# Performance work log

Measured on AMD Instinct MI355X. Metric: run time of the kernel, lower is better.

The kernel has to match this reference:

```python
import jax, jax.numpy as jnp
import numpy as np

N = 4096     # num nodes
FEAT = 500   # knn attribute dim
HID = 512    # args.hid_dim
E = 65536    # edges (avg degree 16)
T = 8        # args.time -> euler steps with step_size=1


def setup_inputs() -> dict:
    key = jax.random.key(0)
    ks = jax.random.split(key, 10)
    knn = jax.random.normal(ks[0], (N, FEAT), jnp.float32)
    adj = jax.random.uniform(ks[1], (N, N), jnp.float32)
    norm_factor = jnp.ones((), jnp.float32)
    edge_index = jax.random.randint(ks[2], (2, E), 0, N, dtype=jnp.int32).astype(jnp.int64)
    edge_weight = jax.random.uniform(ks[3], (E,), jnp.float32)
    # AGCN params (init eye + small noise so math is non-trivial)
    w1 = jnp.eye(N, dtype=jnp.float32) + 0.01 * jax.random.normal(ks[4], (N, N), jnp.float32)
    w2 = jnp.eye(N, dtype=jnp.float32) + 0.01 * jax.random.normal(ks[5], (N, N), jnp.float32)
    # extractor: Linear(N, HID) then Linear(HID, HID), kaiming-normal (relu), zero bias
    W0 = jax.random.normal(ks[6], (HID, N), jnp.float32) * np.float32((2.0 / N) ** 0.5)
    b0 = jnp.zeros((HID,), jnp.float32)
    W1 = jax.random.normal(ks[7], (HID, HID), jnp.float32) * np.float32((2.0 / HID) ** 0.5)
    b1 = jnp.zeros((HID,), jnp.float32)
    # LaplacianODEFunc scalar params
    alpha_train = jnp.asarray(0.5, jnp.float32)
    beta_train = jnp.asarray(0.1, jnp.float32)
    return dict(knn=knn, adj=adj, norm_factor=norm_factor, w1=w1, w2=w2,
                W0=W0, b0=b0, W1=W1, b1=b1, edge_weight=edge_weight,
                alpha_train=alpha_train, beta_train=beta_train, edge_index=edge_index)


def _spmm(edge_index, edge_weight, x):
    # out[row] += w * x[col], row=edge_index[0], col=edge_index[1]
    msg = edge_weight[:, None] * x[edge_index[1]]          # [E, HID]
    return jax.ops.segment_sum(msg, edge_index[0], num_segments=x.shape[0])


def reference(knn, adj, norm_factor, w1, w2, W0, b0, W1, b1,
              edge_weight, alpha_train, beta_train, edge_index):
    # ---- AGCN ----
    H = (adj @ w1) @ adj.T                                  # [N, N]
    H = (H @ w2) @ knn                                      # [N, FEAT]
    embed = H @ H.T                                         # [N, N]
    norm = jnp.maximum(jnp.linalg.norm(embed, axis=1, keepdims=True), 1e-12)
    embed = embed / norm                                    # F.normalize(dim=1)
    # ---- extractor MLP (no activation in source; dropout=eval no-op) ----
    h = embed @ W0.T + b0                                   # [N, HID]
    h = h @ W1.T + b1                                       # [N, HID]
    # ---- ODE diffusion: dx/dt = sigmoid(a)*(Ax - x) + b*x0, explicit Euler dt=1 ----
    x0 = jax.lax.stop_gradient(h)
    alpha = jax.nn.sigmoid(alpha_train)

    def step(x, _):
        ax = _spmm(edge_index, edge_weight, x)
        return x + alpha * (ax - x) + beta_train * x0, None

    z_ode, _ = jax.lax.scan(step, h, None, length=T)
    z = jax.nn.relu(norm_factor * z_ode + h)
    z = (z - z.mean(0)) / jnp.std(z, ddof=1)                # torch std is unbiased
    return z
```

## Files before the change

### kernel.cpp

```cpp
#include <hip/hip_runtime.h>
#include <stdint.h>
#include <stddef.h>

typedef __bf16 bf16;
typedef __attribute__((ext_vector_type(8))) __bf16 bf16x8;
typedef __attribute__((ext_vector_type(4))) __bf16 bf16x4;
typedef __attribute__((ext_vector_type(4))) float f32x4;

#define NN 4096
#define HIDD 512
#define NE 65536

__device__ inline void gll16(const void* g, void* l) {
    __builtin_amdgcn_global_load_lds(
        (const __attribute__((address_space(1))) void*)g,
        (__attribute__((address_space(3))) void*)l, 16, 0, 0);
}

__global__ void cvt_f32_bf16(const float* __restrict__ in, bf16* __restrict__ out, int n) {
    int i = (blockIdx.x * 256 + threadIdx.x) * 4;
    if (i >= n) return;
    float4 v = *reinterpret_cast<const float4*>(in + i);
    bf16x4 o;
    o[0] = (bf16)v.x; o[1] = (bf16)v.y; o[2] = (bf16)v.z; o[3] = (bf16)v.w;
    *reinterpret_cast<bf16x4*>(out + i) = o;
}

__global__ void reduce_bf16_slices(const bf16* __restrict__ in, bf16* __restrict__ out,
                                   int n, int S) {
    int i = (blockIdx.x * 256 + threadIdx.x) * 8;
    if (i >= n) return;
    float acc[8] = {};
    for (int k = 0; k < S; ++k) {
        bf16x8 v = *reinterpret_cast<const bf16x8*>(in + (size_t)k * n + i);
#pragma unroll
        for (int j = 0; j < 8; ++j) acc[j] += (float)v[j];
    }
    bf16x8 o;
#pragma unroll
    for (int j = 0; j < 8; ++j) o[j] = (bf16)acc[j];
    *reinterpret_cast<bf16x8*>(out + i) = o;
}

__global__ void transpose_pad_f32(const float* __restrict__ in, bf16* __restrict__ out,
                                  int R, int C, int Cpad) {
    __shared__ bf16 tile[32][33];
    int c0 = blockIdx.x * 32, r0 = blockIdx.y * 32;
    int tx = threadIdx.x, ty = threadIdx.y;
    for (int i = ty; i < 32; i += 8) {
        int r = r0 + i, c = c0 + tx;
        bf16 v = (bf16)0.f;
        if (r < R && c < C) v = (bf16)in[(size_t)r * C + c];
        tile[i][tx] = v;
    }
    __syncthreads();
    for (int i = ty; i < 32; i += 8) {
        int oc = c0 + i, orow = r0 + tx;
        if (oc < Cpad && orow < R) out[(size_t)oc * R + orow] = tile[tx][i];
    }
}

__global__ void transpose_bf16(const bf16* __restrict__ in, bf16* __restrict__ out,
                               int R, int C) {
    __shared__ bf16 tile[32][33];
    int c0 = blockIdx.x * 32, r0 = blockIdx.y * 32;
    int tx = threadIdx.x, ty = threadIdx.y;
    for (int i = ty; i < 32; i += 8)
        tile[i][tx] = in[(size_t)(r0 + i) * C + c0 + tx];
    __syncthreads();
    for (int i = ty; i < 32; i += 8)
        out[(size_t)(c0 + i) * R + r0 + tx] = tile[tx][i];
}

template<int OMODE, bool HAS_BIAS, bool ROW_SCALE>
__global__ __launch_bounds__(256)
void gemm_nt(const bf16* __restrict__ A, const bf16* __restrict__ B,
             void* __restrict__ Cp, const float* __restrict__ bias,
             const float* __restrict__ rowscale, int M, int N, int K) {
    __shared__ __align__(16) bf16 As[128 * 32];
    __shared__ __align__(16) bf16 Bs[128 * 32];
    const int tid  = threadIdx.x;
    const int wave = tid >> 6;
    const int lane = tid & 63;
    const int m0 = blockIdx.y * 128, n0 = blockIdx.x * 128;
    const int lrow = lane >> 2;
    const int lcol = (lane & 3) * 8;
    const int c0 = wave * 2;
    const size_t arow0 = (size_t)(m0 + c0 * 16 + lrow) * K + lcol;
    const size_t arow1 = (size_t)(m0 + (c0 + 1) * 16 + lrow) * K + lcol;
    const size_t brow0 = (size_t)(n0 + c0 * 16 + lrow) * K + lcol;
    const size_t brow1 = (size_t)(n0 + (c0 + 1) * 16 + lrow) * K + lcol;
    bf16* asd0 = &As[c0 * 512];
    bf16* asd1 = &As[(c0 + 1) * 512];
    bf16* bsd0 = &Bs[c0 * 512];
    bf16* bsd1 = &Bs[(c0 + 1) * 512];

    f32x4 acc[4][4] = {};

    const int wm = (wave >> 1) * 64;
    const int wn = (wave & 1) * 64;
    const int fm = wm + (lane & 15);
    const int fn = wn + (lane & 15);
    const int fk = (lane >> 4) * 8;

    const int kper = K / gridDim.z;
    const int kz0 = blockIdx.z * kper;
    const int kz1 = kz0 + kper;

    for (int k0 = kz0; k0 < kz1; k0 += 32) {
        gll16(A + arow0 + k0, asd0);
        gll16(A + arow1 + k0, asd1);
        gll16(B + brow0 + k0, bsd0);
        gll16(B + brow1 + k0, bsd1);
        __syncthreads();
        bf16x8 af[4], bg[4];
#pragma unroll
        for (int i = 0; i < 4; ++i)
            af[i] = *reinterpret_cast<const bf16x8*>(&As[(fm + i * 16) * 32 + fk]);
#pragma unroll
        for (int j = 0; j < 4; ++j)
            bg[j] = *reinterpret_cast<const bf16x8*>(&Bs[(fn + j * 16) * 32 + fk]);
#pragma unroll
        for (int i = 0; i < 4; ++i)
#pragma unroll
            for (int j = 0; j < 4; ++j)
                acc[i][j] = __builtin_amdgcn_mfma_f32_16x16x32_bf16(af[i], bg[j], acc[i][j], 0, 0, 0);
        __syncthreads();
    }

    const int rbase = m0 + wm + (lane >> 4) * 4;
    const int cbase = n0 + wn + (lane & 15);
    float* outf = (float*)Cp + (size_t)blockIdx.z * M * N;
    bf16*  outb = (bf16*)Cp;
    bf16*  outp = (bf16*)Cp + (size_t)blockIdx.z * M * N;
#pragma unroll
    for (int i = 0; i < 4; ++i) {
#pragma unroll
        for (int j = 0; j < 4; ++j) {
            int col = cbase + j * 16;
            float bv = 0.f;
            if (HAS_BIAS) bv = bias[col];
#pragma unroll
            for (int r = 0; r < 4; ++r) {
                int row = rbase + i * 16 + r;
                float v = acc[i][j][r];
                if (ROW_SCALE) v *= rowscale[row];
                v += bv;
                if (OMODE == 0)      outf[(size_t)row * N + col] = v;
                else if (OMODE == 1) outb[(size_t)row * N + col] = (bf16)v;
                else                 outp[(size_t)row * N + col] = (bf16)v;
            }
        }
    }
}

__global__ void colnorm_part(const bf16* __restrict__ Ht, const float* __restrict__ Rf,
                             float* __restrict__ n2) {
    int i = blockIdx.x * 128 + threadIdx.x;
    int a0 = blockIdx.y * 64;
    float s = 0.f;
    for (int a = a0; a < a0 + 64; ++a)
        s += Rf[(size_t)a * NN + i] * (float)Ht[(size_t)a * NN + i];
    atomicAdd(&n2[i], s);
}

__global__ void colnorm_fin(const float* __restrict__ n2, float* __restrict__ inv) {
    int i = blockIdx.x * 256 + threadIdx.x;
    inv[i] = 1.f / fmaxf(sqrtf(n2[i]), 1e-12f);
}

__global__ void csr_count(const int* __restrict__ ei, int* __restrict__ cnt, int E) {
    int e = blockIdx.x * 256 + threadIdx.x;
    if (e < E) atomicAdd(&cnt[ei[e]], 1);
}

__global__ void scan_4096(const int* __restrict__ cnt, int* __restrict__ rs) {
    __shared__ int s[1024];
    int t = threadIdx.x;
    int b = t * 4;
    int a0 = cnt[b], a1 = cnt[b + 1], a2 = cnt[b + 2], a3 = cnt[b + 3];
    int tot = a0 + a1 + a2 + a3;
    s[t] = tot;
    __syncthreads();
    for (int off = 1; off < 1024; off <<= 1) {
        int v = (t >= off) ? s[t - off] : 0;
        __syncthreads();
        s[t] += v;
        __syncthreads();
    }
    int excl = s[t] - tot;
    rs[b] = excl; rs[b + 1] = excl + a0; rs[b + 2] = excl + a0 + a1; rs[b + 3] = excl + a0 + a1 + a2;
    if (t == 1023) rs[4096] = s[1023];
}

__global__ void csr_scatter(const int* __restrict__ ei, const float* __restrict__ ew,
                            int* __restrict__ cur, int* __restrict__ ccol,
                            float* __restrict__ cw, int E) {
    int e = blockIdx.x * 256 + threadIdx.x;
    if (e < E) {
        int r = ei[e];
        int p = atomicAdd(&cur[r], 1);
        ccol[p] = ei[E + e];
        cw[p] = ew[e];
    }
}

__global__ void ode_step_bf16(const bf16* __restrict__ xin, const bf16* __restrict__ x0,
                              bf16* __restrict__ xout, const int* __restrict__ rs,
                              const int* __restrict__ ccol, const float* __restrict__ cw,
                              const float* __restrict__ alpha_p, const float* __restrict__ beta_p) {
    int row = blockIdx.x * 4 + (threadIdx.x >> 6);
    int lane = threadIdx.x & 63;
    float alpha = 1.f / (1.f + expf(-alpha_p[0]));
    float beta = beta_p[0];
    const bf16x8* xin8 = (const bf16x8*)xin;
    float acc[8] = {};
    int p0 = rs[row], p1 = rs[row + 1];
    for (int p = p0; p < p1; ++p) {
        int c = ccol[p]; float w = cw[p];
        bf16x8 v = xin8[(size_t)c * 64 + lane];
#pragma unroll
        for (int j = 0; j < 8; ++j) acc[j] += w * (float)v[j];
    }
    bf16x8 xi = xin8[(size_t)row * 64 + lane];
    bf16x8 xz = ((const bf16x8*)x0)[(size_t)row * 64 + lane];
    bf16x8 r;
#pragma unroll
    for (int j = 0; j < 8; ++j) {
        float x = (float)xi[j];
        r[j] = (bf16)(x + alpha * (acc[j] - x) + beta * (float)xz[j]);
    }
    ((bf16x8*)xout)[(size_t)row * 64 + lane] = r;
}

__global__ void epi1(const bf16* __restrict__ x8, const bf16* __restrict__ h,
                     const float* __restrict__ nf_p, float* __restrict__ z,
                     float* __restrict__ colsum, float* __restrict__ gst) {
    __shared__ float r1[512], r2[512];
    int b = blockIdx.x, j = threadIdx.x;
    float nf = nf_p[0];
    float cp = 0.f, sq = 0.f;
    for (int i = 0; i < 8; ++i) {
        size_t idx = (size_t)(b * 8 + i) * HIDD + j;
        float v = nf * (float)x8[idx] + (float)h[idx];
        v = fmaxf(v, 0.f);
        z[idx] = v;
        cp += v; sq += v * v;
    }
    atomicAdd(&colsum[j], cp);
    r1[j] = cp; r2[j] = sq;
    __syncthreads();
    for (int off = 256; off > 0; off >>= 1) {
        if (j < off) { r1[j] += r1[j + off]; r2[j] += r2[j + off]; }
        __syncthreads();
    }
    if (j == 0) { atomicAdd(&gst[0], r1[0]); atomicAdd(&gst[1], r2[0]); }
}

__global__ void epi2(const float* __restrict__ z, const float* __restrict__ colsum,
                     const float* __restrict__ gst, float* __restrict__ out) {
    size_t idx = (size_t)blockIdx.x * 256 + threadIdx.x;
    int j = (int)(idx & (HIDD - 1));
    float n = (float)NN * (float)HIDD;
    float gmean = gst[0] / n;
    float var = (gst[1] - n * gmean * gmean) / (n - 1.f);
    float istd = rsqrtf(var);
    float mean = colsum[j] * (1.f / (float)NN);
    out[idx] = (z[idx] - mean) * istd;
}

extern "C" void kernel_launch(void* const* d_in, const int* in_sizes, int n_in,
                              void* d_out, int out_size, void* d_ws, size_t ws_size,
                              hipStream_t stream) {
    const float* knn  = (const float*)d_in[0];
    const float* adj  = (const float*)d_in[1];
    const float* nf   = (const float*)d_in[2];
    const float* w1   = (const float*)d_in[3];
    const float* w2   = (const float*)d_in[4];
    const float* W0   = (const float*)d_in[5];
    const float* b0   = (const float*)d_in[6];
    const float* W1   = (const float*)d_in[7];
    const float* b1   = (const float*)d_in[8];
    const float* ew   = (const float*)d_in[9];
    const float* alph = (const float*)d_in[10];
    const float* beta = (const float*)d_in[11];
    const int*   ei   = (const int*)d_in[12];

    char* w = (char*)d_ws;
    size_t off = 0;
    auto alloc = [&](size_t bytes) -> char* {
        char* p = w + off;
        off += (bytes + 255) & ~(size_t)255;
        return p;
    };
    const size_t SZ_NN  = (size_t)NN * NN * sizeof(bf16);
    const size_t SZ_TH  = (size_t)HIDD * NN * sizeof(bf16);
    bf16* Bar  = (bf16*)alloc(SZ_NN);
    bf16* Car  = (bf16*)alloc(SZ_NN);
    bf16* knnT = (bf16*)alloc(SZ_TH);
    bf16* tA   = (bf16*)alloc(SZ_TH);
    bf16* tB   = (bf16*)alloc(SZ_TH);
    float* tf  = (float*)alloc((size_t)16 * 1024 * 1024);
    bf16* Hm   = (bf16*)alloc(SZ_TH);
    bf16* Gb   = (bf16*)alloc((size_t)HIDD * HIDD * sizeof(bf16));
    bf16* M0tb = (bf16*)alloc((size_t)HIDD * HIDD * sizeof(bf16));
    bf16* h1b  = (bf16*)alloc((size_t)NN * HIDD * sizeof(bf16));
    bf16* hb   = (bf16*)alloc((size_t)NN * HIDD * sizeof(bf16));
    float* inv = (float*)alloc(NN * sizeof(float));
    float* n2  = (float*)alloc(NN * sizeof(float));
    int*  cnt  = (int*)alloc(NN * sizeof(int));
    int*  rs   = (int*)alloc((NN + 1) * sizeof(int));
    int*  cur  = (int*)alloc(NN * sizeof(int));
    int*  ccol = (int*)alloc(NE * sizeof(int));
    float* cw  = (float*)alloc(NE * sizeof(float));
    float* colsum = (float*)alloc(HIDD * sizeof(float));
    float* gst = (float*)alloc(2 * sizeof(float));
    bf16* tfb = (bf16*)tf;
    bf16* W1b = (bf16*)((char*)Car + 16 * 1024 * 1024);
    bf16* xA  = (bf16*)Car;
    bf16* xB  = (bf16*)Car + (size_t)NN * HIDD;
    (void)ws_size; (void)n_in; (void)in_sizes; (void)out_size;

    dim3 tb(32, 8);
    const int nTH = HIDD * NN;
    const int nHH = HIDD * HIDD;

    transpose_pad_f32<<<dim3(16, 128), tb, 0, stream>>>(knn, knnT, NN, 500, HIDD);
    cvt_f32_bf16<<<(NN * NN) / 1024, 256, 0, stream>>>(w2, Car, NN * NN);
    transpose_pad_f32<<<dim3(128, 128), tb, 0, stream>>>(adj, Bar, NN, NN, NN);

    gemm_nt<2, false, false><<<dim3(32, 4, 4), 256, 0, stream>>>(knnT, Car, tfb, nullptr, nullptr, HIDD, NN, NN);
    reduce_bf16_slices<<<nTH / 2048, 256, 0, stream>>>(tfb, tA, nTH, 4);
    gemm_nt<2, false, false><<<dim3(32, 4, 4), 256, 0, stream>>>(tA, Bar, tfb, nullptr, nullptr, HIDD, NN, NN);
    reduce_bf16_slices<<<nTH / 2048, 256, 0, stream>>>(tfb, tB, nTH, 4);
    cvt_f32_bf16<<<(NN * NN) / 1024, 256, 0, stream>>>(w1, Car, NN * NN);
    gemm_nt<2, false, false><<<dim3(32, 4, 4), 256, 0, stream>>>(tB, Car, tfb, nullptr, nullptr, HIDD, NN, NN);
    reduce_bf16_slices<<<nTH / 2048, 256, 0, stream>>>(tfb, tA, nTH, 4);
    cvt_f32_bf16<<<(NN * NN) / 1024, 256, 0, stream>>>(adj, Bar, NN * NN);
    gemm_nt<2, false, false><<<dim3(32, 4, 4), 256, 0, stream>>>(tA, Bar, tfb, nullptr, nullptr, HIDD, NN, NN);
    reduce_bf16_slices<<<nTH / 2048, 256, 0, stream>>>(tfb, tB, nTH, 4);

    transpose_bf16<<<dim3(128, 16), tb, 0, stream>>>(tB, Hm, HIDD, NN);

    gemm_nt<2, false, false><<<dim3(4, 4, 16), 256, 0, stream>>>(tB, tB, tfb, nullptr, nullptr, HIDD, HIDD, NN);
    reduce_bf16_slices<<<nHH / 2048, 256, 0, stream>>>(tfb, Gb, nHH, 16);

    gemm_nt<0, false, false><<<dim3(32, 4, 1), 256, 0, stream>>>(Gb, Hm, tf, nullptr, nullptr, HIDD, NN, HIDD);
    hipMemsetAsync(n2, 0, NN * sizeof(float), stream);
    colnorm_part<<<dim3(32, 8), 128, 0, stream>>>(tB, tf, n2);
    colnorm_fin<<<NN / 256, 256, 0, stream>>>(n2, inv);

    cvt_f32_bf16<<<(HIDD * NN) / 1024, 256, 0, stream>>>(W0, Car, HIDD * NN);
    gemm_nt<2, false, false><<<dim3(4, 4, 16), 256, 0, stream>>>(Car, tB, tfb, nullptr, nullptr, HIDD, HIDD, NN);
    reduce_bf16_slices<<<nHH / 2048, 256, 0, stream>>>(tfb, M0tb, nHH, 16);

    gemm_nt<1, true, true><<<dim3(4, 32, 1), 256, 0, stream>>>(Hm, M0tb, h1b, b0, inv, NN, HIDD, HIDD);
    cvt_f32_bf16<<<(HIDD * HIDD) / 1024, 256, 0, stream>>>(W1, W1b, HIDD * HIDD);
    gemm_nt<1, true, false><<<dim3(4, 32, 1), 256, 0, stream>>>(h1b, W1b, hb, b1, nullptr, NN, HIDD, HIDD);

    hipMemsetAsync(cnt, 0, NN * sizeof(int), stream);
    csr_count<<<NE / 256, 256, 0, stream>>>(ei, cnt, NE);
    scan_4096<<<1, 1024, 0, stream>>>(cnt, rs);
    hipMemcpyAsync(cur, rs, NN * sizeof(int), hipMemcpyDeviceToDevice, stream);
    csr_scatter<<<NE / 256, 256, 0, stream>>>(ei, ew, cur, ccol, cw, NE);

    const bf16* xi = hb;
    bf16* xo = xA;
    for (int s = 0; s < 8; ++s) {
        ode_step_bf16<<<NN / 4, 256, 0, stream>>>(xi, hb, xo, rs, ccol, cw, alph, beta);
        xi = xo;
        xo = (s % 2 == 0) ? xB : xA;
    }

    hipMemsetAsync(colsum, 0, HIDD * sizeof(float), stream);
    hipMemsetAsync(gst, 0, 2 * sizeof(float), stream);
    epi1<<<NN / 8, 512, 0, stream>>>(xB, hb, nf, tf, colsum, gst);
    epi2<<<(NN * HIDD) / 256, 256, 0, stream>>>(tf, colsum, gst, (float*)d_out);
}
```

Baseline: 675.5 us.

## Fuse fp32-to-bf16 conversion into GEMM B loads and raise split-K

The GEMM gains a mode that reads fp32 B directly from global memory, converts it to bf16 in registers and stores it to LDS. This removes the separate full-matrix conversion passes for w1, w2 and adj, and a faster 64x64 vectorized transpose replaces the 32x32 one for adjT. Split-K goes from 4 to 8 slices on the big GEMMs, and the small NxHID GEMMs now use split-K of 2, with bias and row-scale moved into a new reduce kernel. The trade-off is more partial-sum traffic and synchronous fp32 loads that no longer use the direct-to-LDS path.

After: 691.7 us. 1.02x slower.

```diff
diff --git a/kernel.cpp b/kernel.cpp
--- a/kernel.cpp
+++ b/kernel.cpp
@@ -39,6 +39,30 @@
     bf16x8 o;
 #pragma unroll
     for (int j = 0; j < 8; ++j) o[j] = (bf16)acc[j];
+    *reinterpret_cast<bf16x8*>(out + i) = o;
+}
+
+template<bool RS>
+__global__ void reduce_affine512(const bf16* __restrict__ in, bf16* __restrict__ out,
+                                 int S, const float* __restrict__ rs,
+                                 const float* __restrict__ bias) {
+    int i = (blockIdx.x * 256 + threadIdx.x) * 8;
+    const int n = NN * HIDD;
+    float acc[8] = {};
+    for (int k = 0; k < S; ++k) {
+        bf16x8 v = *reinterpret_cast<const bf16x8*>(in + (size_t)k * n + i);
+#pragma unroll
+        for (int j = 0; j < 8; ++j) acc[j] += (float)v[j];
+    }
+    int col = i & (HIDD - 1);
+    int row = i >> 9;
+    float scale = RS ? rs[row] : 1.f;
+    float4 bA = *reinterpret_cast<const float4*>(bias + col);
+    float4 bB = *reinterpret_cast<const float4*>(bias + col + 4);
+    float bb[8] = {bA.x, bA.y, bA.z, bA.w, bB.x, bB.y, bB.z, bB.w};
+    bf16x8 o;
+#pragma unroll
+    for (int j = 0; j < 8; ++j) o[j] = (bf16)(acc[j] * scale + bb[j]);
     *reinterpret_cast<bf16x8*>(out + i) = o;
 }
 
@@ -60,6 +84,32 @@
     }
 }
 
+__global__ __launch_bounds__(256)
+void transpose64_f32_bf16(const float* __restrict__ in, bf16* __restrict__ out,
+                          int R, int C) {
+    __shared__ bf16 tile[64][66];
+    int c0 = blockIdx.x * 64, r0 = blockIdx.y * 64;
+    int tx = threadIdx.x & 15, ty = threadIdx.x >> 4;
+#pragma unroll
+    for (int rr = 0; rr < 4; ++rr) {
+        int r = ty + rr * 16;
+        float4 v = *reinterpret_cast<const float4*>(in + (size_t)(r0 + r) * C + c0 + tx * 4);
+        tile[r][tx * 4 + 0] = (bf16)v.x;
+        tile[r][tx * 4 + 1] = (bf16)v.y;
+        tile[r][tx * 4 + 2] = (bf16)v.z;
+        tile[r][tx * 4 + 3] = (bf16)v.w;
+    }
+    __syncthreads();
+#pragma unroll
+    for (int cc = 0; cc < 4; ++cc) {
+        int c = ty + cc * 16;
+        bf16x4 o;
+#pragma unroll
+        for (int j = 0; j < 4; ++j) o[j] = tile[tx * 4 + j][c];
+        *reinterpret_cast<bf16x4*>(out + (size_t)(c0 + c) * R + r0 + tx * 4) = o;
+    }
+}
+
 __global__ void transpose_bf16(const bf16* __restrict__ in, bf16* __restrict__ out,
                                int R, int C) {
     __shared__ bf16 tile[32][33];
@@ -72,11 +122,10 @@
         out[(size_t)(c0 + i) * R + r0 + tx] = tile[tx][i];
 }
 
-template<int OMODE, bool HAS_BIAS, bool ROW_SCALE>
+template<int OMODE, bool BF32>
 __global__ __launch_bounds__(256)
-void gemm_nt(const bf16* __restrict__ A, const bf16* __restrict__ B,
-             void* __restrict__ Cp, const float* __restrict__ bias,
-             const float* __restrict__ rowscale, int M, int N, int K) {
+void gemm_nt(const bf16* __restrict__ A, const void* __restrict__ Bv,
+             void* __restrict__ Cp, int M, int N, int K) {
     __shared__ __align__(16) bf16 As[128 * 32];
     __shared__ __align__(16) bf16 Bs[128 * 32];
     const int tid  = threadIdx.x;
@@ -94,6 +143,11 @@
     bf16* asd1 = &As[(c0 + 1) * 512];
     bf16* bsd0 = &Bs[c0 * 512];
     bf16* bsd1 = &Bs[(c0 + 1) * 512];
+    const bf16*  Bb = (const bf16*)Bv;
+    const float* Bf = (const float*)Bv;
+    const int trow  = tid >> 1;
+    const int khalf = (tid & 1) * 16;
+    const size_t bfrow = (size_t)(n0 + trow) * K + khalf;
 
     f32x4 acc[4][4] = {};
 
@@ -110,8 +164,23 @@
     for (int k0 = kz0; k0 < kz1; k0 += 32) {
         gll16(A + arow0 + k0, asd0);
         gll16(A + arow1 + k0, asd1);
-        gll16(B + brow0 + k0, bsd0);
-        gll16(B + brow1 + k0, bsd1);
+        if (BF32) {
+            const float* src = Bf + bfrow + k0;
+            float4 v0 = *reinterpret_cast<const float4*>(src + 0);
+            float4 v1 = *reinterpret_cast<const float4*>(src + 4);
+            float4 v2 = *reinterpret_cast<const float4*>(src + 8);
+            float4 v3 = *reinterpret_cast<const float4*>(src + 12);
+            bf16x8 p0, p1;
+            p0[0] = (bf16)v0.x; p0[1] = (bf16)v0.y; p0[2] = (bf16)v0.z; p0[3] = (bf16)v0.w;
+            p0[4] = (bf16)v1.x; p0[5] = (bf16)v1.y; p0[6] = (bf16)v1.z; p0[7] = (bf16)v1.w;
+            p1[0] = (bf16)v2.x; p1[1] = (bf16)v2.y; p1[2] = (bf16)v2.z; p1[3] = (bf16)v2.w;
+            p1[4] = (bf16)v3.x; p1[5] = (bf16)v3.y; p1[6] = (bf16)v3.z; p1[7] = (bf16)v3.w;
+            *reinterpret_cast<bf16x8*>(&Bs[trow * 32 + khalf]) = p0;
+            *reinterpret_cast<bf16x8*>(&Bs[trow * 32 + khalf + 8]) = p1;
+        } else {
+            gll16(Bb + brow0 + k0, bsd0);
+            gll16(Bb + brow1 + k0, bsd1);
+        }
         __syncthreads();
         bf16x8 af[4], bg[4];
 #pragma unroll
@@ -138,14 +207,10 @@
 #pragma unroll
         for (int j = 0; j < 4; ++j) {
             int col = cbase + j * 16;
-            float bv = 0.f;
-            if (HAS_BIAS) bv = bias[col];
 #pragma unroll
             for (int r = 0; r < 4; ++r) {
                 int row = rbase + i * 16 + r;
                 float v = acc[i][j][r];
-                if (ROW_SCALE) v *= rowscale[row];
-                v += bv;
                 if (OMODE == 0)      outf[(size_t)row * N + col] = v;
                 else if (OMODE == 1) outb[(size_t)row * N + col] = (bf16)v;
                 else                 outp[(size_t)row * N + col] = (bf16)v;
@@ -154,13 +219,14 @@
     }
 }
 
-__global__ void colnorm_part(const bf16* __restrict__ Ht, const float* __restrict__ Rf,
-                             float* __restrict__ n2) {
+__global__ void colnorm_part2(const bf16* __restrict__ Ht, const float* __restrict__ Rf,
+                              float* __restrict__ n2) {
     int i = blockIdx.x * 128 + threadIdx.x;
     int a0 = blockIdx.y * 64;
+    const float* R1 = Rf + (size_t)HIDD * NN;
     float s = 0.f;
     for (int a = a0; a < a0 + 64; ++a)
-        s += Rf[(size_t)a * NN + i] * (float)Ht[(size_t)a * NN + i];
+        s += (Rf[(size_t)a * NN + i] + R1[(size_t)a * NN + i]) * (float)Ht[(size_t)a * NN + i];
     atomicAdd(&n2[i], s);
 }
 
@@ -293,32 +359,32 @@
         off += (bytes + 255) & ~(size_t)255;
         return p;
     };
-    const size_t SZ_NN  = (size_t)NN * NN * sizeof(bf16);
-    const size_t SZ_TH  = (size_t)HIDD * NN * sizeof(bf16);
-    bf16* Bar  = (bf16*)alloc(SZ_NN);
-    bf16* Car  = (bf16*)alloc(SZ_NN);
-    bf16* knnT = (bf16*)alloc(SZ_TH);
-    bf16* tA   = (bf16*)alloc(SZ_TH);
-    bf16* tB   = (bf16*)alloc(SZ_TH);
-    float* tf  = (float*)alloc((size_t)16 * 1024 * 1024);
-    bf16* Hm   = (bf16*)alloc(SZ_TH);
-    bf16* Gb   = (bf16*)alloc((size_t)HIDD * HIDD * sizeof(bf16));
-    bf16* M0tb = (bf16*)alloc((size_t)HIDD * HIDD * sizeof(bf16));
-    bf16* h1b  = (bf16*)alloc((size_t)NN * HIDD * sizeof(bf16));
-    bf16* hb   = (bf16*)alloc((size_t)NN * HIDD * sizeof(bf16));
-    float* inv = (float*)alloc(NN * sizeof(float));
-    float* n2  = (float*)alloc(NN * sizeof(float));
-    int*  cnt  = (int*)alloc(NN * sizeof(int));
-    int*  rs   = (int*)alloc((NN + 1) * sizeof(int));
-    int*  cur  = (int*)alloc(NN * sizeof(int));
-    int*  ccol = (int*)alloc(NE * sizeof(int));
-    float* cw  = (float*)alloc(NE * sizeof(float));
+    const size_t SZ_NN = (size_t)NN * NN * sizeof(bf16);
+    const size_t SZ_TH = (size_t)HIDD * NN * sizeof(bf16);
+    bf16*  adjT = (bf16*)alloc(SZ_NN);
+    bf16*  Par  = (bf16*)alloc(SZ_NN);
+    bf16*  knnT = (bf16*)alloc(SZ_TH);
+    bf16*  tA   = (bf16*)alloc(SZ_TH);
+    bf16*  tB   = (bf16*)alloc(SZ_TH);
+    bf16*  Hm   = (bf16*)alloc(SZ_TH);
+    bf16*  W0b  = (bf16*)alloc(SZ_TH);
+    bf16*  h1b  = (bf16*)alloc((size_t)NN * HIDD * sizeof(bf16));
+    bf16*  hb   = (bf16*)alloc((size_t)NN * HIDD * sizeof(bf16));
+    bf16*  xA   = (bf16*)alloc((size_t)NN * HIDD * sizeof(bf16));
+    bf16*  xB   = (bf16*)alloc((size_t)NN * HIDD * sizeof(bf16));
+    bf16*  Gb   = (bf16*)alloc((size_t)HIDD * HIDD * sizeof(bf16));
+    bf16*  M0tb = (bf16*)alloc((size_t)HIDD * HIDD * sizeof(bf16));
+    bf16*  W1b  = (bf16*)alloc((size_t)HIDD * HIDD * sizeof(bf16));
+    float* inv  = (float*)alloc(NN * sizeof(float));
+    float* n2   = (float*)alloc(NN * sizeof(float));
+    int*   cnt  = (int*)alloc(NN * sizeof(int));
+    int*   rs   = (int*)alloc((NN + 1) * sizeof(int));
+    int*   cur  = (int*)alloc(NN * sizeof(int));
+    int*   ccol = (int*)alloc(NE * sizeof(int));
+    float* cw   = (float*)alloc(NE * sizeof(float));
     float* colsum = (float*)alloc(HIDD * sizeof(float));
-    float* gst = (float*)alloc(2 * sizeof(float));
-    bf16* tfb = (bf16*)tf;
-    bf16* W1b = (bf16*)((char*)Car + 16 * 1024 * 1024);
-    bf16* xA  = (bf16*)Car;
-    bf16* xB  = (bf16*)Car + (size_t)NN * HIDD;
+    float* gst  = (float*)alloc(2 * sizeof(float));
+    float* Parf = (float*)Par;
     (void)ws_size; (void)n_in; (void)in_sizes; (void)out_size;
 
     dim3 tb(32, 8);
@@ -326,37 +392,36 @@
     const int nHH = HIDD * HIDD;
 
     transpose_pad_f32<<<dim3(16, 128), tb, 0, stream>>>(knn, knnT, NN, 500, HIDD);
-    cvt_f32_bf16<<<(NN * NN) / 1024, 256, 0, stream>>>(w2, Car, NN * NN);
-    transpose_pad_f32<<<dim3(128, 128), tb, 0, stream>>>(adj, Bar, NN, NN, NN);
-
-    gemm_nt<2, false, false><<<dim3(32, 4, 4), 256, 0, stream>>>(knnT, Car, tfb, nullptr, nullptr, HIDD, NN, NN);
-    reduce_bf16_slices<<<nTH / 2048, 256, 0, stream>>>(tfb, tA, nTH, 4);
-    gemm_nt<2, false, false><<<dim3(32, 4, 4), 256, 0, stream>>>(tA, Bar, tfb, nullptr, nullptr, HIDD, NN, NN);
-    reduce_bf16_slices<<<nTH / 2048, 256, 0, stream>>>(tfb, tB, nTH, 4);
-    cvt_f32_bf16<<<(NN * NN) / 1024, 256, 0, stream>>>(w1, Car, NN * NN);
-    gemm_nt<2, false, false><<<dim3(32, 4, 4), 256, 0, stream>>>(tB, Car, tfb, nullptr, nullptr, HIDD, NN, NN);
-    reduce_bf16_slices<<<nTH / 2048, 256, 0, stream>>>(tfb, tA, nTH, 4);
-    cvt_f32_bf16<<<(NN * NN) / 1024, 256, 0, stream>>>(adj, Bar, NN * NN);
-    gemm_nt<2, false, false><<<dim3(32, 4, 4), 256, 0, stream>>>(tA, Bar, tfb, nullptr, nullptr, HIDD, NN, NN);
-    reduce_bf16_slices<<<nTH / 2048, 256, 0, stream>>>(tfb, tB, nTH, 4);
+    transpose64_f32_bf16<<<dim3(64, 64), 256, 0, stream>>>(adj, adjT, NN, NN);
+
+    gemm_nt<2, true ><<<dim3(32, 4, 8), 256, 0, stream>>>(knnT, w2,   Par, HIDD, NN, NN);
+    reduce_bf16_slices<<<nTH / 2048, 256, 0, stream>>>(Par, tA, nTH, 8);
+    gemm_nt<2, false><<<dim3(32, 4, 8), 256, 0, stream>>>(tA,   adjT, Par, HIDD, NN, NN);
+    reduce_bf16_slices<<<nTH / 2048, 256, 0, stream>>>(Par, tB, nTH, 8);
+    gemm_nt<2, true ><<<dim3(32, 4, 8), 256, 0, stream>>>(tB,   w1,   Par, HIDD, NN, NN);
+    reduce_bf16_slices<<<nTH / 2048, 256, 0, stream>>>(Par, tA, nTH, 8);
+    gemm_nt<2, true ><<<dim3(32, 4, 8), 256, 0, stream>>>(tA,   adj,  Par, HIDD, NN, NN);
+    reduce_bf16_slices<<<nTH / 2048, 256, 0, stream>>>(Par, tB, nTH, 8);
 
     transpose_bf16<<<dim3(128, 16), tb, 0, stream>>>(tB, Hm, HIDD, NN);
 
-    gemm_nt<2, false, false><<<dim3(4, 4, 16), 256, 0, stream>>>(tB, tB, tfb, nullptr, nullptr, HIDD, HIDD, NN);
-    reduce_bf16_slices<<<nHH / 2048, 256, 0, stream>>>(tfb, Gb, nHH, 16);
-
-    gemm_nt<0, false, false><<<dim3(32, 4, 1), 256, 0, stream>>>(Gb, Hm, tf, nullptr, nullptr, HIDD, NN, HIDD);
+    gemm_nt<2, false><<<dim3(4, 4, 16), 256, 0, stream>>>(tB, tB, Par, HIDD, HIDD, NN);
+    reduce_bf16_slices<<<nHH / 2048, 256, 0, stream>>>(Par, Gb, nHH, 16);
+
+    gemm_nt<0, false><<<dim3(32, 4, 2), 256, 0, stream>>>(Gb, Hm, Parf, HIDD, NN, HIDD);
     hipMemsetAsync(n2, 0, NN * sizeof(float), stream);
-    colnorm_part<<<dim3(32, 8), 128, 0, stream>>>(tB, tf, n2);
+    colnorm_part2<<<dim3(32, 8), 128, 0, stream>>>(tB, Parf, n2);
     colnorm_fin<<<NN / 256, 256, 0, stream>>>(n2, inv);
 
-    cvt_f32_bf16<<<(HIDD * NN) / 1024, 256, 0, stream>>>(W0, Car, HIDD * NN);
-    gemm_nt<2, false, false><<<dim3(4, 4, 16), 256, 0, stream>>>(Car, tB, tfb, nullptr, nullptr, HIDD, HIDD, NN);
-    reduce_bf16_slices<<<nHH / 2048, 256, 0, stream>>>(tfb, M0tb, nHH, 16);
-
-    gemm_nt<1, true, true><<<dim3(4, 32, 1), 256, 0, stream>>>(Hm, M0tb, h1b, b0, inv, NN, HIDD, HIDD);
+    cvt_f32_bf16<<<(HIDD * NN) / 1024, 256, 0, stream>>>(W0, W0b, HIDD * NN);
+    gemm_nt<2, false><<<dim3(4, 4, 16), 256, 0, stream>>>(W0b, tB, Par, HIDD, HIDD, NN);
+    reduce_bf16_slices<<<nHH / 2048, 256, 0, stream>>>(Par, M0tb, nHH, 16);
+
+    gemm_nt<2, false><<<dim3(4, 32, 2), 256, 0, stream>>>(Hm, M0tb, Par, NN, HIDD, HIDD);
+    reduce_affine512<true><<<nTH / 2048, 256, 0, stream>>>(Par, h1b, 2, inv, b0);
     cvt_f32_bf16<<<(HIDD * HIDD) / 1024, 256, 0, stream>>>(W1, W1b, HIDD * HIDD);
-    gemm_nt<1, true, false><<<dim3(4, 32, 1), 256, 0, stream>>>(h1b, W1b, hb, b1, nullptr, NN, HIDD, HIDD);
+    gemm_nt<2, false><<<dim3(4, 32, 2), 256, 0, stream>>>(h1b, W1b, Par, NN, HIDD, HIDD);
+    reduce_affine512<false><<<nTH / 2048, 256, 0, stream>>>(Par, hb, 2, nullptr, b1);
 
     hipMemsetAsync(cnt, 0, NN * sizeof(int), stream);
     csr_count<<<NE / 256, 256, 0, stream>>>(ei, cnt, NE);
@@ -374,6 +439,6 @@
 
     hipMemsetAsync(colsum, 0, HIDD * sizeof(float), stream);
     hipMemsetAsync(gst, 0, 2 * sizeof(float), stream);
-    epi1<<<NN / 8, 512, 0, stream>>>(xB, hb, nf, tf, colsum, gst);
-    epi2<<<(NN * HIDD) / 256, 256, 0, stream>>>(tf, colsum, gst, (float*)d_out);
-}
+    epi1<<<NN / 8, 512, 0, stream>>>(xB, hb, nf, Parf, colsum, gst);
+    epi2<<<(NN * HIDD) / 256, 256, 0, stream>>>(Parf, colsum, gst, (float*)d_out);
+}
```
